# Performance work log

Hardware: AMD Instinct MI355X
Metric: run time of the kernel (lower is better)

Reference implementation:

```python
import jax, jax.numpy as jnp
import numpy as np

N, E = 50000, 800000
MUL, NATTR, NEMB, HID, NPATH = 32, 8, 8, 8, 5
AVG_NEIGH = 16.0
INV3 = 1.0 / np.sqrt(3.0)  # CG norm for 1o x 1o -> 0e (dot)
INV2 = 1.0 / np.sqrt(2.0)  # CG norm for 1o x 1o -> 1o (cross)


def setup_inputs() -> dict:
    key = jax.random.key(0)
    ks = jax.random.split(key, 16)
    f = lambda k, s: jax.random.normal(k, s, jnp.float32)
    return {
        "node_s": f(ks[0], (N, MUL)),
        "node_v": f(ks[1], (N, MUL, 3)),
        "node_attrs": f(ks[2], (N, NATTR)),
        "edge_emb": f(ks[3], (E, NEMB)),
        "edge_sh0": f(ks[4], (E, 1)),
        "edge_sh1": f(ks[5], (E, 3)),
        "W1_s": f(ks[6], (MUL, MUL)),
        "W1_v": f(ks[7], (MUL, MUL)),
        "Wm1": f(ks[8], (NEMB, HID)),
        "Wm2": f(ks[9], (HID, NPATH * MUL)),
        "W2_s": f(ks[10], (2 * MUL, MUL)),
        "W2_v": f(ks[11], (3 * MUL, MUL)),
        "Wsc_s": f(ks[12], (MUL, NATTR, MUL)),
        "Wsc_v": f(ks[13], (MUL, NATTR, MUL)),
        "edge_src": jax.random.randint(ks[14], (E,), 0, N),
        "edge_dst": jax.random.randint(ks[15], (E,), 0, N),
    }


def reference(node_s, node_v, node_attrs, edge_emb, edge_sh0, edge_sh1,
              W1_s, W1_v, Wm1, Wm2, W2_s, W2_v, Wsc_s, Wsc_v,
              edge_src, edge_dst):
    # linear_1: per-l equivariant channel mixing
    x_s = node_s @ W1_s / np.sqrt(MUL)                          # [N, MUL]
    x_v = jnp.einsum('nuc,uv->nvc', node_v, W1_v) / np.sqrt(MUL)  # [N, MUL, 3]
    # gather source node features per edge
    s = x_s[edge_src]   # [E, MUL]
    v = x_v[edge_src]   # [E, MUL, 3]
    # radial MLP on edge embedding -> per-edge UVU tensor-product weights
    h = jax.nn.silu(edge_emb @ Wm1 / np.sqrt(NEMB))
    w = (h @ Wm2 / np.sqrt(HID)).reshape(E, NPATH, MUL)
    w1, w2, w3, w4, w5 = (w[:, i] for i in range(NPATH))
    # UVU Clebsch-Gordan paths (lmax = 1)
    p1 = w1 * s * edge_sh0                                              # 0e x 0e -> 0e
    p2 = w2 * jnp.einsum('euc,ec->eu', v, edge_sh1) * INV3              # 1o x 1o -> 0e
    p3 = w3[:, :, None] * s[:, :, None] * edge_sh1[:, None, :]          # 0e x 1o -> 1o
    p4 = w4[:, :, None] * v * edge_sh0[:, :, None]                      # 1o x 0e -> 1o
    p5 = w5[:, :, None] * jnp.cross(v, edge_sh1[:, None, :]) * INV2     # 1o x 1o -> 1o
    msg_s = jnp.concatenate([p1, p2], axis=1)       # [E, 2*MUL]
    msg_v = jnp.concatenate([p3, p4, p5], axis=1)   # [E, 3*MUL, 3]
    # scatter-add messages to destination nodes
    agg_s = jax.ops.segment_sum(msg_s, edge_dst, num_segments=N)
    agg_v = jax.ops.segment_sum(msg_v, edge_dst, num_segments=N)
    inv = 1.0 / np.sqrt(AVG_NEIGH)
    agg_s = agg_s * inv
    agg_v = agg_v * inv
    # linear_2
    m_s = agg_s @ W2_s / np.sqrt(2 * MUL)
    m_v = jnp.einsum('nuc,uv->nvc', agg_v, W2_v) / np.sqrt(3 * MUL)
    # self connection: fully connected TP with scalar node attrs
    nsc = 1.0 / np.sqrt(MUL * NATTR)
    sc_s = jnp.einsum('nu,na,uav->nv', node_s, node_attrs, Wsc_s) * nsc
    sc_v = jnp.einsum('nuc,na,uav->nvc', node_v, node_attrs, Wsc_v) * nsc
    out_s = m_s + sc_s                  # [N, MUL]
    out_v = m_v + sc_v                  # [N, MUL, 3]
    return jnp.concatenate([out_s, out_v.reshape(N, MUL * 3)], axis=1)  # [N, 128]
```

## Files before the change

### kernel.cpp

```cpp
#include <hip/hip_runtime.h>
#include <math.h>

#define NN 50000
#define NE 800000
#define MUL 32
#define CHUNK 16
#define SCANB 49

static __device__ __forceinline__ float sigmoidf_(float v) {
    return 1.0f / (1.0f + __expf(-v));
}

#define INV_SQRT_MUL   0.17677669529663687f
#define INV_SQRT_NEMB  0.35355339059327373f
#define INV_SQRT_HID   0.35355339059327373f
#define INV3C          0.5773502691896258f
#define INV2C          0.7071067811865476f
#define INV_NEIGH      0.25f
#define INV_SQRT_2MUL  0.125f
#define INV_SQRT_3MUL  0.10206207261596575f
#define NSC            0.0625f

__global__ __launch_bounds__(256) void k_node(
    const float* __restrict__ node_s, const float* __restrict__ node_v,
    const float* __restrict__ attrs,
    const float* __restrict__ W1_s, const float* __restrict__ W1_v,
    const float* __restrict__ Wsc_s, const float* __restrict__ Wsc_v,
    float* __restrict__ x, float* __restrict__ out)
{
    __shared__ float nd[2][136];
    __shared__ float gs[2][1024];
    __shared__ float gv[2][1024];
    const int t  = threadIdx.x;
    const int h  = t >> 7;
    const int tl = t & 127;
    const int n  = blockIdx.x * 2 + h;

    if (tl < 32) nd[h][tl] = node_s[n * 32 + tl];
    else         nd[h][tl] = node_v[n * 96 + (tl - 32)];
    if (tl < 8)  nd[h][128 + tl] = attrs[n * 8 + tl];
    __syncthreads();

    float at[8];
#pragma unroll
    for (int a = 0; a < 8; ++a) at[a] = nd[h][128 + a];

#pragma unroll
    for (int r = 0; r < 8; ++r) {
        int idx = tl + 128 * r;
        int u = idx >> 5, vch = idx & 31;
        float as = 0.f, av = 0.f;
#pragma unroll
        for (int a = 0; a < 8; ++a) {
            as += at[a] * Wsc_s[(u * 8 + a) * 32 + vch];
            av += at[a] * Wsc_v[(u * 8 + a) * 32 + vch];
        }
        gs[h][idx] = as;
        gv[h][idx] = av;
    }
    __syncthreads();

    float xa = 0.f, sc = 0.f;
    if (tl < 32) {
#pragma unroll
        for (int u = 0; u < 32; ++u) {
            xa += nd[h][u] * W1_s[u * 32 + tl];
            sc += nd[h][u] * gs[h][(u << 5) + tl];
        }
    } else {
        int q = tl - 32;
        int vch = q / 3, c = q - 3 * vch;
#pragma unroll
        for (int u = 0; u < 32; ++u) {
            float vv = nd[h][32 + u * 3 + c];
            xa += vv * W1_v[u * 32 + vch];
            sc += vv * gv[h][(u << 5) + vch];
        }
    }
    x[n * 128 + tl]   = xa * INV_SQRT_MUL;
    out[n * 128 + tl] = sc * NSC;
}

__global__ __launch_bounds__(256) void k_hist(
    const int* __restrict__ edge_dst, int* __restrict__ counts)
{
    int e = blockIdx.x * 256 + threadIdx.x;
    if (e >= NE) return;
    atomicAdd(&counts[edge_dst[e]], 1);
}

__global__ __launch_bounds__(1024) void k_scan_a(
    const int* __restrict__ counts, int* __restrict__ escan,
    int* __restrict__ bsum)
{
    __shared__ int sh[1024];
    const int t = threadIdx.x;
    const int i = blockIdx.x * 1024 + t;
    int v = (i < NN) ? counts[i] : 0;
    sh[t] = v;
    __syncthreads();
    for (int off = 1; off < 1024; off <<= 1) {
        int u = (t >= off) ? sh[t - off] : 0;
        __syncthreads();
        sh[t] += u;
        __syncthreads();
    }
    if (i < NN) escan[i] = sh[t] - v;
    if (t == 1023) bsum[blockIdx.x] = sh[1023];
}

__global__ __launch_bounds__(64) void k_scan_b(int* __restrict__ bsum)
{
    const int t = threadIdx.x;
    int v = (t < SCANB) ? bsum[t] : 0;
    const int orig = v;
    for (int off = 1; off < 64; off <<= 1) {
        int u = __shfl_up(v, off, 64);
        if (t >= off) v += u;
    }
    if (t < SCANB) bsum[t] = v - orig;
}

__global__ __launch_bounds__(1024) void k_scan_c(
    const int* __restrict__ escan, const int* __restrict__ bsum,
    int* __restrict__ offsets, int* __restrict__ cursor)
{
    const int i = blockIdx.x * 1024 + threadIdx.x;
    if (i == 0) offsets[NN] = NE;
    if (i < NN) {
        int o = bsum[blockIdx.x] + escan[i];
        offsets[i] = o;
        cursor[i] = o;
    }
}

__global__ __launch_bounds__(256) void k_pack(
    const float* __restrict__ edge_emb, const float* __restrict__ edge_sh0,
    const float* __restrict__ edge_sh1,
    const int* __restrict__ edge_src, const int* __restrict__ edge_dst,
    const float* __restrict__ Wm1,
    int* __restrict__ cursor, float* __restrict__ epack)
{
    int e = blockIdx.x * 256 + threadIdx.x;
    if (e >= NE) return;
    const float4* p = (const float4*)(edge_emb + e * 8);
    float4 a = p[0], b = p[1];
    float emb[8] = {a.x, a.y, a.z, a.w, b.x, b.y, b.z, b.w};
    float h[8];
#pragma unroll
    for (int j = 0; j < 8; ++j) {
        float s = 0.f;
#pragma unroll
        for (int k = 0; k < 8; ++k) s += emb[k] * Wm1[k * 8 + j];
        s *= INV_SQRT_NEMB;
        h[j] = s * sigmoidf_(s);
    }
    float sh0 = edge_sh0[e];
    float sx = edge_sh1[3 * e], sy = edge_sh1[3 * e + 1], sz = edge_sh1[3 * e + 2];
    int src = edge_src[e];
    int pos = atomicAdd(&cursor[edge_dst[e]], 1);
    float4* op = (float4*)(epack + (size_t)pos * 16);
    op[0] = make_float4(__int_as_float(src), sh0, sx, sy);
    op[1] = make_float4(sz, h[0], h[1], h[2]);
    op[2] = make_float4(h[3], h[4], h[5], h[6]);
    op[3] = make_float4(h[7], 0.f, 0.f, 0.f);
}

__global__ __launch_bounds__(64) void k_gather(
    const float* __restrict__ x, const float* __restrict__ epack,
    const float* __restrict__ Wm2, const float* __restrict__ W2_s,
    const float* __restrict__ W2_v,
    const int* __restrict__ offsets, float* __restrict__ out)
{
    __shared__ float meta[CHUNK * 16];
    __shared__ float msg[352];
    const int n = blockIdx.x;
    const int L = threadIdx.x;
    const int u = L & 31;
    const int role = L >> 5;

    float wc[3][8];
#pragma unroll
    for (int p = 0; p < 3; ++p) {
        int m = (role == 0 ? p : 3 + p) * 32 + u;
        if (m > 159) m = u;
#pragma unroll
        for (int q = 0; q < 8; ++q) wc[p][q] = Wm2[q * 160 + m];
    }

    float a0 = 0.f, a1 = 0.f;
    float b0 = 0.f, b1 = 0.f, b2 = 0.f;
    float c0 = 0.f, c1 = 0.f, c2 = 0.f;

    const int beg = offsets[n];
    const int end = offsets[n + 1];

    for (int base = beg; base < end; base += CHUNK) {
        const int cnt = min(CHUNK, end - base);
        {
            int ee = L >> 2;
            if (ee < cnt) {
                float4 v = ((const float4*)epack)[(size_t)(base + ee) * 4 + (L & 3)];
                *(float4*)&meta[ee * 16 + 4 * (L & 3)] = v;
            }
        }
        __syncthreads();

        float ls, lv0, lv1, lv2;
        {
            const float* xr = x + (size_t)__float_as_int(meta[0]) * 128;
            ls  = xr[u];
            lv0 = xr[32 + 3 * u]; lv1 = xr[33 + 3 * u]; lv2 = xr[34 + 3 * u];
        }
        for (int jj = 0; jj < cnt; ++jj) {
            float ns = 0.f, nv0 = 0.f, nv1 = 0.f, nv2 = 0.f;
            if (jj + 1 < cnt) {
                const float* xr = x + (size_t)__float_as_int(meta[(jj + 1) * 16]) * 128;
                ns  = xr[u];
                nv0 = xr[32 + 3 * u]; nv1 = xr[33 + 3 * u]; nv2 = xr[34 + 3 * u];
            }
            const float* mp = &meta[jj * 16];
            const float sh0 = mp[1], sx = mp[2], sy = mp[3], sz = mp[4];
            float w0 = 0.f, w1 = 0.f, w2 = 0.f;
#pragma unroll
            for (int q = 0; q < 8; ++q) {
                float hq = mp[5 + q];
                w0 += hq * wc[0][q];
                w1 += hq * wc[1][q];
                w2 += hq * wc[2][q];
            }
            w0 *= INV_SQRT_HID; w1 *= INV_SQRT_HID; w2 *= INV_SQRT_HID;
            if (role == 0) {
                a0 += w0 * ls * sh0;
                float dot = lv0 * sx + lv1 * sy + lv2 * sz;
                a1 += w1 * dot;
                float t = w2 * ls;
                b0 += t * sx; b1 += t * sy; b2 += t * sz;
            } else {
                float t4 = w0 * sh0;
                b0 += t4 * lv0; b1 += t4 * lv1; b2 += t4 * lv2;
                float cx = lv1 * sz - lv2 * sy;
                float cy = lv2 * sx - lv0 * sz;
                float cz = lv0 * sy - lv1 * sx;
                c0 += w1 * cx; c1 += w1 * cy; c2 += w1 * cz;
            }
            ls = ns; lv0 = nv0; lv1 = nv1; lv2 = nv2;
        }
        __syncthreads();
    }

    if (role == 0) {
        msg[u]      = a0 * INV_NEIGH;
        msg[32 + u] = a1 * (INV3C * INV_NEIGH);
        int vb = 64 + u * 3;
        msg[vb]     = b0 * INV_NEIGH;
        msg[vb + 1] = b1 * INV_NEIGH;
        msg[vb + 2] = b2 * INV_NEIGH;
    } else {
        int vb4 = 64 + (32 + u) * 3;
        msg[vb4]     = b0 * INV_NEIGH;
        msg[vb4 + 1] = b1 * INV_NEIGH;
        msg[vb4 + 2] = b2 * INV_NEIGH;
        int vb5 = 64 + (64 + u) * 3;
        float f = INV2C * INV_NEIGH;
        msg[vb5]     = c0 * f;
        msg[vb5 + 1] = c1 * f;
        msg[vb5 + 2] = c2 * f;
    }
    __syncthreads();

#pragma unroll
    for (int oo = 0; oo < 2; ++oo) {
        int o = oo * 64 + L;
        float r;
        if (o < 32) {
            float s = 0.f;
#pragma unroll
            for (int uu = 0; uu < 64; ++uu) s += msg[uu] * W2_s[uu * 32 + o];
            r = s * INV_SQRT_2MUL;
        } else {
            int q = o - 32;
            int vch = q / 3, c = q - 3 * vch;
            float s = 0.f;
#pragma unroll
            for (int uu = 0; uu < 96; ++uu) s += msg[64 + uu * 3 + c] * W2_v[uu * 32 + vch];
            r = s * INV_SQRT_3MUL;
        }
        out[128 * n + o] += r;
    }
}

extern "C" void kernel_launch(void* const* d_in, const int* in_sizes, int n_in,
                              void* d_out, int out_size, void* d_ws, size_t ws_size,
                              hipStream_t stream) {
    const float* node_s   = (const float*)d_in[0];
    const float* node_v   = (const float*)d_in[1];
    const float* attrs    = (const float*)d_in[2];
    const float* edge_emb = (const float*)d_in[3];
    const float* edge_sh0 = (const float*)d_in[4];
    const float* edge_sh1 = (const float*)d_in[5];
    const float* W1_s     = (const float*)d_in[6];
    const float* W1_v     = (const float*)d_in[7];
    const float* Wm1      = (const float*)d_in[8];
    const float* Wm2      = (const float*)d_in[9];
    const float* W2_s     = (const float*)d_in[10];
    const float* W2_v     = (const float*)d_in[11];
    const float* Wsc_s    = (const float*)d_in[12];
    const float* Wsc_v    = (const float*)d_in[13];
    const int*   edge_src = (const int*)d_in[14];
    const int*   edge_dst = (const int*)d_in[15];
    float* out = (float*)d_out;

    float* x     = (float*)d_ws;
    float* epack = x + (size_t)NN * 128;
    int*   counts  = (int*)(epack + (size_t)NE * 16);
    int*   offsets = counts + NN;
    int*   cursor  = offsets + NN + 1;
    int*   escan   = cursor + NN;
    int*   bsum    = escan + NN;

    hipMemsetAsync(counts, 0, NN * sizeof(int), stream);

    k_node<<<NN / 2, 256, 0, stream>>>(node_s, node_v, attrs,
                                       W1_s, W1_v, Wsc_s, Wsc_v, x, out);
    k_hist<<<(NE + 255) / 256, 256, 0, stream>>>(edge_dst, counts);
    k_scan_a<<<SCANB, 1024, 0, stream>>>(counts, escan, bsum);
    k_scan_b<<<1, 64, 0, stream>>>(bsum);
    k_scan_c<<<SCANB, 1024, 0, stream>>>(escan, bsum, offsets, cursor);
    k_pack<<<(NE + 255) / 256, 256, 0, stream>>>(edge_emb, edge_sh0, edge_sh1,
                                                 edge_src, edge_dst, Wm1,
                                                 cursor, epack);
    k_gather<<<NN, 64, 0, stream>>>(x, epack, Wm2, W2_s, W2_v, offsets, out);
}
```

Before: 499.0 us.

## Split gather edges across two wavefronts and pre-transpose linear_2 weights

```diff
diff --git a/kernel.cpp b/kernel.cpp
--- a/kernel.cpp
+++ b/kernel.cpp
@@ -134,6 +134,21 @@
     }
 }
 
+__global__ __launch_bounds__(256) void k_prep(
+    const float* __restrict__ W2_s, const float* __restrict__ W2_v,
+    float* __restrict__ W2T_s, float* __restrict__ W2T_v)
+{
+    int t = blockIdx.x * 256 + threadIdx.x;
+    if (t < 2048) {
+        int o = t >> 6, uu = t & 63;
+        W2T_s[t] = W2_s[uu * 32 + o] * INV_SQRT_2MUL;
+    }
+    if (t < 3072) {
+        int vch = t / 96, uu = t - vch * 96;
+        W2T_v[t] = W2_v[uu * 32 + vch] * INV_SQRT_3MUL;
+    }
+}
+
 __global__ __launch_bounds__(256) void k_pack(
     const float* __restrict__ edge_emb, const float* __restrict__ edge_sh0,
     const float* __restrict__ edge_sh1,
@@ -160,24 +175,27 @@
     int src = edge_src[e];
     int pos = atomicAdd(&cursor[edge_dst[e]], 1);
     float4* op = (float4*)(epack + (size_t)pos * 16);
-    op[0] = make_float4(__int_as_float(src), sh0, sx, sy);
-    op[1] = make_float4(sz, h[0], h[1], h[2]);
-    op[2] = make_float4(h[3], h[4], h[5], h[6]);
-    op[3] = make_float4(h[7], 0.f, 0.f, 0.f);
-}
-
-__global__ __launch_bounds__(64) void k_gather(
+    op[0] = make_float4(sh0, sx, sy, sz);
+    op[1] = make_float4(__int_as_float(src), 0.f, 0.f, 0.f);
+    op[2] = make_float4(h[0], h[1], h[2], h[3]);
+    op[3] = make_float4(h[4], h[5], h[6], h[7]);
+}
+
+__global__ __launch_bounds__(128) void k_gather(
     const float* __restrict__ x, const float* __restrict__ epack,
-    const float* __restrict__ Wm2, const float* __restrict__ W2_s,
-    const float* __restrict__ W2_v,
+    const float* __restrict__ Wm2,
+    const float* __restrict__ W2T_s, const float* __restrict__ W2T_v,
     const int* __restrict__ offsets, float* __restrict__ out)
 {
-    __shared__ float meta[CHUNK * 16];
-    __shared__ float msg[352];
+    __shared__ float meta[2][CHUNK * 16];
+    __shared__ float msg_s[64];
+    __shared__ float mver[288];
     const int n = blockIdx.x;
     const int L = threadIdx.x;
-    const int u = L & 31;
-    const int role = L >> 5;
+    const int wv = L >> 6;
+    const int lane = L & 63;
+    const int u = lane & 31;
+    const int role = lane >> 5;
 
     float wc[3][8];
 #pragma unroll
@@ -185,7 +203,7 @@
         int m = (role == 0 ? p : 3 + p) * 32 + u;
         if (m > 159) m = u;
 #pragma unroll
-        for (int q = 0; q < 8; ++q) wc[p][q] = Wm2[q * 160 + m];
+        for (int q = 0; q < 8; ++q) wc[p][q] = Wm2[q * 160 + m] * INV_SQRT_HID;
     }
 
     float a0 = 0.f, a1 = 0.f;
@@ -194,42 +212,51 @@
 
     const int beg = offsets[n];
     const int end = offsets[n + 1];
-
-    for (int base = beg; base < end; base += CHUNK) {
-        const int cnt = min(CHUNK, end - base);
+    const int total = end - beg;
+    const int halfc = (total + 1) >> 1;
+    const int wbeg = beg + wv * halfc;
+    const int wend = wv ? end : (beg + halfc);
+    float* mt = meta[wv];
+
+    for (int cb = wbeg; cb < wend; cb += CHUNK) {
+        const int cnt = min(CHUNK, wend - cb);
         {
-            int ee = L >> 2;
-            if (ee < cnt) {
-                float4 v = ((const float4*)epack)[(size_t)(base + ee) * 4 + (L & 3)];
-                *(float4*)&meta[ee * 16 + 4 * (L & 3)] = v;
+            int rec = lane >> 2;
+            if (rec < cnt) {
+                float4 v = ((const float4*)epack)[(size_t)(cb + rec) * 4 + (lane & 3)];
+                *(float4*)&mt[rec * 16 + 4 * (lane & 3)] = v;
             }
         }
-        __syncthreads();
 
         float ls, lv0, lv1, lv2;
         {
-            const float* xr = x + (size_t)__float_as_int(meta[0]) * 128;
+            int src_s = __builtin_amdgcn_readfirstlane(__float_as_int(mt[4]));
+            const float* xr = x + (size_t)src_s * 128;
             ls  = xr[u];
             lv0 = xr[32 + 3 * u]; lv1 = xr[33 + 3 * u]; lv2 = xr[34 + 3 * u];
         }
         for (int jj = 0; jj < cnt; ++jj) {
             float ns = 0.f, nv0 = 0.f, nv1 = 0.f, nv2 = 0.f;
             if (jj + 1 < cnt) {
-                const float* xr = x + (size_t)__float_as_int(meta[(jj + 1) * 16]) * 128;
+                int src_s = __builtin_amdgcn_readfirstlane(
+                    __float_as_int(mt[(jj + 1) * 16 + 4]));
+                const float* xr = x + (size_t)src_s * 128;
                 ns  = xr[u];
                 nv0 = xr[32 + 3 * u]; nv1 = xr[33 + 3 * u]; nv2 = xr[34 + 3 * u];
             }
-            const float* mp = &meta[jj * 16];
-            const float sh0 = mp[1], sx = mp[2], sy = mp[3], sz = mp[4];
+            float4 shv = *(const float4*)&mt[jj * 16];
+            float4 h0v = *(const float4*)&mt[jj * 16 + 8];
+            float4 h1v = *(const float4*)&mt[jj * 16 + 12];
+            const float sh0 = shv.x, sx = shv.y, sy = shv.z, sz = shv.w;
+            float hq[8] = {h0v.x, h0v.y, h0v.z, h0v.w,
+                           h1v.x, h1v.y, h1v.z, h1v.w};
             float w0 = 0.f, w1 = 0.f, w2 = 0.f;
 #pragma unroll
             for (int q = 0; q < 8; ++q) {
-                float hq = mp[5 + q];
-                w0 += hq * wc[0][q];
-                w1 += hq * wc[1][q];
-                w2 += hq * wc[2][q];
+                w0 += hq[q] * wc[0][q];
+                w1 += hq[q] * wc[1][q];
+                w2 += hq[q] * wc[2][q];
             }
-            w0 *= INV_SQRT_HID; w1 *= INV_SQRT_HID; w2 *= INV_SQRT_HID;
             if (role == 0) {
                 a0 += w0 * ls * sh0;
                 float dot = lv0 * sx + lv1 * sy + lv2 * sz;
@@ -246,48 +273,67 @@
             }
             ls = ns; lv0 = nv0; lv1 = nv1; lv2 = nv2;
         }
-        __syncthreads();
-    }
-
-    if (role == 0) {
-        msg[u]      = a0 * INV_NEIGH;
-        msg[32 + u] = a1 * (INV3C * INV_NEIGH);
-        int vb = 64 + u * 3;
-        msg[vb]     = b0 * INV_NEIGH;
-        msg[vb + 1] = b1 * INV_NEIGH;
-        msg[vb + 2] = b2 * INV_NEIGH;
+    }
+
+    __syncthreads();
+    if (wv == 0) {
+        if (role == 0) {
+            msg_s[u]      = a0 * INV_NEIGH;
+            msg_s[32 + u] = a1 * (INV3C * INV_NEIGH);
+            mver[u]       = b0 * INV_NEIGH;
+            mver[96 + u]  = b1 * INV_NEIGH;
+            mver[192 + u] = b2 * INV_NEIGH;
+        } else {
+            mver[32 + u]       = b0 * INV_NEIGH;
+            mver[96 + 32 + u]  = b1 * INV_NEIGH;
+            mver[192 + 32 + u] = b2 * INV_NEIGH;
+            float f = INV2C * INV_NEIGH;
+            mver[64 + u]       = c0 * f;
+            mver[96 + 64 + u]  = c1 * f;
+            mver[192 + 64 + u] = c2 * f;
+        }
+    }
+    __syncthreads();
+    if (wv == 1) {
+        if (role == 0) {
+            msg_s[u]      += a0 * INV_NEIGH;
+            msg_s[32 + u] += a1 * (INV3C * INV_NEIGH);
+            mver[u]       += b0 * INV_NEIGH;
+            mver[96 + u]  += b1 * INV_NEIGH;
+            mver[192 + u] += b2 * INV_NEIGH;
+        } else {
+            mver[32 + u]       += b0 * INV_NEIGH;
+            mver[96 + 32 + u]  += b1 * INV_NEIGH;
+            mver[192 + 32 + u] += b2 * INV_NEIGH;
+            float f = INV2C * INV_NEIGH;
+            mver[64 + u]       += c0 * f;
+            mver[96 + 64 + u]  += c1 * f;
+            mver[192 + 64 + u] += c2 * f;
+        }
+    }
+    __syncthreads();
+
+    float acc = 0.f;
+    if (L < 32) {
+        const float4* w4 = (const float4*)(W2T_s + L * 64);
+        const float4* m4 = (const float4*)msg_s;
+#pragma unroll
+        for (int g = 0; g < 16; ++g) {
+            float4 w = w4[g], m = m4[g];
+            acc += w.x * m.x + w.y * m.y + w.z * m.z + w.w * m.w;
+        }
     } else {
-        int vb4 = 64 + (32 + u) * 3;
-        msg[vb4]     = b0 * INV_NEIGH;
-        msg[vb4 + 1] = b1 * INV_NEIGH;
-        msg[vb4 + 2] = b2 * INV_NEIGH;
-        int vb5 = 64 + (64 + u) * 3;
-        float f = INV2C * INV_NEIGH;
-        msg[vb5]     = c0 * f;
-        msg[vb5 + 1] = c1 * f;
-        msg[vb5 + 2] = c2 * f;
-    }
-    __syncthreads();
-
-#pragma unroll
-    for (int oo = 0; oo < 2; ++oo) {
-        int o = oo * 64 + L;
-        float r;
-        if (o < 32) {
-            float s = 0.f;
-#pragma unroll
-            for (int uu = 0; uu < 64; ++uu) s += msg[uu] * W2_s[uu * 32 + o];
-            r = s * INV_SQRT_2MUL;
-        } else {
-            int q = o - 32;
-            int vch = q / 3, c = q - 3 * vch;
-            float s = 0.f;
-#pragma unroll
-            for (int uu = 0; uu < 96; ++uu) s += msg[64 + uu * 3 + c] * W2_v[uu * 32 + vch];
-            r = s * INV_SQRT_3MUL;
-        }
-        out[128 * n + o] += r;
-    }
+        int q = L - 32;
+        int vch = q / 3, c = q - 3 * vch;
+        const float4* w4 = (const float4*)(W2T_v + vch * 96);
+        const float4* m4 = (const float4*)(mver + c * 96);
+#pragma unroll
+        for (int g = 0; g < 24; ++g) {
+            float4 w = w4[g], m = m4[g];
+            acc += w.x * m.x + w.y * m.y + w.z * m.z + w.w * m.w;
+        }
+    }
+    out[128 * n + L] += acc;
 }
 
 extern "C" void kernel_launch(void* const* d_in, const int* in_sizes, int n_in,
@@ -318,6 +364,8 @@
     int*   cursor  = offsets + NN + 1;
     int*   escan   = cursor + NN;
     int*   bsum    = escan + NN;
+    float* W2T_s   = (float*)(bsum + SCANB + 1);
+    float* W2T_v   = W2T_s + 2048;
 
     hipMemsetAsync(counts, 0, NN * sizeof(int), stream);
 
@@ -327,8 +375,10 @@
     k_scan_a<<<SCANB, 1024, 0, stream>>>(counts, escan, bsum);
     k_scan_b<<<1, 64, 0, stream>>>(bsum);
     k_scan_c<<<SCANB, 1024, 0, stream>>>(escan, bsum, offsets, cursor);
+    k_prep<<<12, 256, 0, stream>>>(W2_s, W2_v, W2T_s, W2T_v);
     k_pack<<<(NE + 255) / 256, 256, 0, stream>>>(edge_emb, edge_sh0, edge_sh1,
                                                  edge_src, edge_dst, Wm1,
                                                  cursor, epack);
-    k_gather<<<NN, 64, 0, stream>>>(x, epack, Wm2, W2_s, W2_v, offsets, out);
-}
+    k_gather<<<NN, 128, 0, stream>>>(x, epack, Wm2, W2T_s, W2T_v,
+                                     offsets, out);
+}
```

After: 591.0 us. 1.18x slower.
